# Optimization experiments

Measured on AMD Instinct MI355X. Metric: run time of the kernel, lower is better.

## Reference

```python
import jax, jax.numpy as jnp
import numpy as np

NODE_DIM, HIDDEN, PROJ = 5, 128, 256
NUM_MP = 3
BOX = 1.0


def _knn_edges(positions, k, box_length=BOX):
    """Periodic kNN graph. positions: (B,N,3) -> (src, dst) global flat indices, E = B*N*k."""
    B, N, _ = positions.shape

    def per_batch(pos):  # (N,3)
        delta = jnp.abs(pos[:, None, :] - pos[None, :, :])          # (N,N,3)
        delta = jnp.where(delta > 0.5 * box_length, box_length - delta, delta)
        dist = jnp.sqrt(jnp.sum(delta * delta, axis=-1) + 1e-12)    # (N,N)
        _, idx = jax.lax.top_k(-dist, k + 1)                        # k+1 smallest
        return idx[:, 1:]                                           # drop self -> (N,k)

    nbrs = jax.vmap(per_batch)(positions)                           # (B,N,k)
    offset = (jnp.arange(B) * N)[:, None, None]
    src = jnp.broadcast_to(jnp.arange(N)[None, :, None], (B, N, k)) + offset
    dst = nbrs + offset
    return src.reshape(-1), dst.reshape(-1)


def setup_inputs() -> dict:
    key = jax.random.key(0)
    ks = jax.random.split(key, 16)
    B, N = 8, 2048
    s = 0.05
    inp = {
        "x": jax.random.normal(ks[0], (B, N, NODE_DIM), jnp.float32),
        "positions": jax.random.uniform(ks[1], (B, N, 3), jnp.float32),
        "k": 16,
        # encoder: Linear(5,128)+ReLU, Linear(128,128)+ReLU
        "enc_w0": jax.random.normal(ks[2], (NODE_DIM, HIDDEN), jnp.float32) * s,
        "enc_b0": jnp.zeros((HIDDEN,), jnp.float32),
        "enc_w1": jax.random.normal(ks[3], (HIDDEN, HIDDEN), jnp.float32) * s,
        "enc_b1": jnp.zeros((HIDDEN,), jnp.float32),
        # message nets: Linear(2H,H)+ReLU per round
        "msg_w": jax.random.normal(ks[4], (NUM_MP, 2 * HIDDEN, HIDDEN), jnp.float32) * s,
        "msg_b": jnp.zeros((NUM_MP, HIDDEN), jnp.float32),
        # update nets: Linear(2H,H)+ReLU per round
        "upd_w": jax.random.normal(ks[5], (NUM_MP, 2 * HIDDEN, HIDDEN), jnp.float32) * s,
        "upd_b": jnp.zeros((NUM_MP, HIDDEN), jnp.float32),
        # projection head: Linear(H,H)+ReLU, Linear(H,proj)
        "proj_w0": jax.random.normal(ks[6], (HIDDEN, HIDDEN), jnp.float32) * s,
        "proj_b0": jnp.zeros((HIDDEN,), jnp.float32),
        "proj_w1": jax.random.normal(ks[7], (HIDDEN, PROJ), jnp.float32) * s,
        "proj_b1": jnp.zeros((PROJ,), jnp.float32),
    }
    return inp


def reference(x, positions, k, enc_w0, enc_b0, enc_w1, enc_b1,
              msg_w, msg_b, upd_w, upd_b, proj_w0, proj_b0, proj_w1, proj_b1):
    B, N, _ = x.shape
    BN = B * N
    relu = jax.nn.relu

    # encoder over flattened nodes
    h = relu(x.reshape(BN, -1) @ enc_w0 + enc_b0)
    h = relu(h @ enc_w1 + enc_b1)

    src, dst = _knn_edges(positions, k)
    E = src.shape[0]
    deg = jax.ops.segment_sum(jnp.ones((E,), h.dtype), dst, num_segments=BN)
    inv_deg = 1.0 / jnp.clip(deg, 1.0)

    for i in range(NUM_MP):
        # per-edge message: concat(sender, receiver) -> Linear+ReLU
        msg = relu(jnp.concatenate([h[src], h[dst]], axis=-1) @ msg_w[i] + msg_b[i])
        # mean aggregation at destination nodes
        agg = jax.ops.segment_sum(msg, dst, num_segments=BN) * inv_deg[:, None]
        # residual update
        h = h + relu(jnp.concatenate([h, agg], axis=-1) @ upd_w[i] + upd_b[i])

    z = relu(h @ proj_w0 + proj_b0) @ proj_w1 + proj_b1
    return z.reshape(B, N, PROJ), h.reshape(B, N, HIDDEN)
```

## Files before the change

kernel.cpp:

```cpp
#include <hip/hip_runtime.h>
#include <stdint.h>
#include <math.h>

#define NN 2048
#define BB 8
#define BN (BB*NN)
#define KK 16
#define EE (BN*KK)
#define HID 128
#define PROJ_D 256
#define QPB 16
#define CDIM 6
#define NCELL (CDIM*CDIM*CDIM)
#define CAP 768

typedef unsigned long long u64;
typedef unsigned short ushort_t;
typedef __attribute__((ext_vector_type(8))) short short8;
typedef __attribute__((ext_vector_type(4))) float f32x4;

__device__ __forceinline__ u64 wave_min_u64(u64 v) {
  #pragma unroll
  for (int off = 32; off > 0; off >>= 1) {
    u64 o = __shfl_xor(v, off);
    v = o < v ? o : v;
  }
  return v;
}

__global__ __launch_bounds__(256) void cellsort_kernel(
    const float* __restrict__ pos, float4* __restrict__ spos,
    int* __restrict__ cptr, int4* __restrict__ cntz) {
  __shared__ int hist[NCELL];
  __shared__ int base[NCELL];
  const int b = blockIdx.x, tid = threadIdx.x;
  #pragma unroll
  for (int k = 0; k < 4; k++)
    cntz[(b * 256 + tid) + k * 2048] = make_int4(0, 0, 0, 0);
  if (tid < NCELL) hist[tid] = 0;
  __syncthreads();
  int cellv[8];
  float4 pv[8];
  #pragma unroll
  for (int k = 0; k < 8; k++) {
    int j = tid * 8 + k;
    const float* pp = pos + ((size_t)b * NN + j) * 3;
    float x = pp[0], y = pp[1], z = pp[2];
    int cx = (int)(x * 6.0f); cx = cx > 5 ? 5 : cx;
    int cy = (int)(y * 6.0f); cy = cy > 5 ? 5 : cy;
    int cz = (int)(z * 6.0f); cz = cz > 5 ? 5 : cz;
    int cell = (cx * 6 + cy) * 6 + cz;
    cellv[k] = cell;
    pv[k] = make_float4(x, y, z, __int_as_float(j));
    atomicAdd(&hist[cell], 1);
  }
  __syncthreads();
  if (tid == 0) {
    int run = 0;
    for (int c = 0; c < NCELL; c++) {
      cptr[b * (NCELL + 1) + c] = run;
      base[c] = run;
      run += hist[c];
    }
    cptr[b * (NCELL + 1) + NCELL] = run;
  }
  __syncthreads();
  if (tid < NCELL) hist[tid] = 0;
  __syncthreads();
  #pragma unroll
  for (int k = 0; k < 8; k++) {
    int slot = base[cellv[k]] + atomicAdd(&hist[cellv[k]], 1);
    spos[(size_t)b * NN + slot] = pv[k];
  }
}

__global__ __launch_bounds__(1024) void knn_kernel(
    const float4* __restrict__ spos, const int* __restrict__ cptr,
    int* __restrict__ nbr, int* __restrict__ cnt) {
  __shared__ float4 Ps[NN];
  __shared__ unsigned Hist[QPB * 256];
  __shared__ ushort_t Cand[QPB * CAP];
  __shared__ int Cp[NCELL + 1];
  const int b  = blockIdx.x >> 7;
  const int qb = blockIdx.x & 127;
  const int wave = threadIdx.x >> 6;
  const int lane = threadIdx.x & 63;
  const int s_q = qb * QPB + wave;

  for (int t = threadIdx.x; t < NN; t += 1024)
    Ps[t] = spos[(size_t)b * NN + t];
  if (threadIdx.x <= NCELL)
    Cp[threadIdx.x] = cptr[b * (NCELL + 1) + threadIdx.x];
  __syncthreads();

  const float4 q = Ps[s_q];
  const float xi = q.x, yi = q.y, zi = q.z;
  const int orig_i = __float_as_int(q.w);
  unsigned* H = &Hist[wave * 256];
  ushort_t* CL = &Cand[wave * CAP];

  int cx = (int)(xi * 6.0f); cx = cx > 5 ? 5 : cx;
  int cy = (int)(yi * 6.0f); cy = cy > 5 ? 5 : cy;
  int cz = (int)(zi * 6.0f); cz = cz > 5 ? 5 : cz;

  int T = 0;
  bool ovf = false;
  #pragma unroll 1
  for (int dxy = 0; dxy < 9; dxy++) {
    int dx = dxy / 3 - 1, dy = dxy - (dxy / 3) * 3 - 1;
    int ncx = cx + dx; ncx += (ncx < 0) ? 6 : 0; ncx -= (ncx >= 6) ? 6 : 0;
    int ncy = cy + dy; ncy += (ncy < 0) ? 6 : 0; ncy -= (ncy >= 6) ? 6 : 0;
    int cbse = (ncx * 6 + ncy) * 6;
    int s0, l0, s1 = 0, l1 = 0;
    if (cz == 0) {
      s0 = Cp[cbse + 5]; l0 = Cp[cbse + 6] - s0;
      s1 = Cp[cbse];     l1 = Cp[cbse + 2] - s1;
    } else if (cz == 5) {
      s0 = Cp[cbse + 4]; l0 = Cp[cbse + 6] - s0;
      s1 = Cp[cbse];     l1 = Cp[cbse + 1] - s1;
    } else {
      s0 = Cp[cbse + cz - 1]; l0 = Cp[cbse + cz + 2] - s0;
    }
    if (T + l0 + l1 > CAP) { ovf = true; break; }
    for (int t = lane; t < l0; t += 64) CL[T + t] = (ushort_t)(s0 + t);
    T += l0;
    for (int t = lane; t < l1; t += 64) CL[T + t] = (ushort_t)(s1 + t);
    T += l1;
  }

  int mode = ovf ? 1 : 0;
  float scale = 1536.0f;
  int T2 = T, binmax = 254;
  int bstar = 0; unsigned C = 0;
  for (;;) {
    scale = mode ? 256.0f : 1536.0f;
    T2 = mode ? NN : T;
    binmax = mode ? 256 : 254;
    *(uint4*)&H[lane * 4] = make_uint4(0u, 0u, 0u, 0u);
    for (int t = lane; t < T2; t += 64) {
      int p = mode ? t : (int)CL[t];
      float4 pj = Ps[p];
      float tx = xi - pj.x, ty = yi - pj.y, tz = zi - pj.z;
      float ddx = __fsub_rn(tx, rintf(tx));
      float ddy = __fsub_rn(ty, rintf(ty));
      float ddz = __fsub_rn(tz, rintf(tz));
      float s = __fadd_rn(__fadd_rn(__fadd_rn(__fmul_rn(ddx,ddx), __fmul_rn(ddy,ddy)),
                                    __fmul_rn(ddz,ddz)), 1e-12f);
      float d = __fsqrt_rn(s);
      int bin = (int)(d * scale);
      if (bin < binmax) atomicAdd(&H[bin], 1u);
    }
    uint4 cv = *(const uint4*)&H[lane * 4];
    unsigned s4 = cv.x + cv.y + cv.z + cv.w;
    unsigned incl = s4;
    #pragma unroll
    for (int off = 1; off < 64; off <<= 1) {
      unsigned v = __shfl_up(incl, off);
      if (lane >= off) incl += v;
    }
    unsigned total = __shfl(incl, 63);
    if (total >= 17u) {
      unsigned base = incl - s4;
      bool has = (incl >= 17u) && (base < 17u);
      u64 hmask = __ballot(has);
      int srcl = __ffsll((unsigned long long)hmask) - 1;
      int bl = 0; unsigned Cl = 0;
      if (has) {
        if (base + cv.x >= 17u)                    { bl = lane*4 + 0; Cl = base; }
        else if (base + cv.x + cv.y >= 17u)        { bl = lane*4 + 1; Cl = base + cv.x; }
        else if (base + cv.x + cv.y + cv.z >= 17u) { bl = lane*4 + 2; Cl = base + cv.x + cv.y; }
        else                                       { bl = lane*4 + 3; Cl = base + cv.x + cv.y + cv.z; }
      }
      bstar = __shfl(bl, srcl);
      C     = __shfl(Cl, srcl);
      break;
    }
    mode = 1;
  }
  const int m = 17 - (int)C;

  u64 lst[6];
  #pragma unroll
  for (int t = 0; t < 6; t++) lst[t] = ~0ull;
  for (int t = lane; t < T2; t += 64) {
    int p = mode ? t : (int)CL[t];
    float4 pj = Ps[p];
    float tx = xi - pj.x, ty = yi - pj.y, tz = zi - pj.z;
    float ddx = __fsub_rn(tx, rintf(tx));
    float ddy = __fsub_rn(ty, rintf(ty));
    float ddz = __fsub_rn(tz, rintf(tz));
    float s = __fadd_rn(__fadd_rn(__fadd_rn(__fmul_rn(ddx,ddx), __fmul_rn(ddy,ddy)),
                                  __fmul_rn(ddz,ddz)), 1e-12f);
    float d = __fsqrt_rn(s);
    int bin = (int)(d * scale);
    if (bin == bstar) {
      u64 key = ((u64)__float_as_uint(d) << 11) | (unsigned)__float_as_int(pj.w);
      if (key < lst[5]) {
        lst[5] = key;
        #pragma unroll
        for (int u = 5; u > 0; u--) {
          u64 a = lst[u-1], c2 = lst[u];
          lst[u-1] = a < c2 ? a : c2;
          lst[u]   = a < c2 ? c2 : a;
        }
      }
    }
  }

  u64 kstar = 0;
  #pragma unroll 1
  for (int r = 0; r < m; r++) {
    u64 h0 = lst[0];
    u64 gm = wave_min_u64(h0);
    kstar = gm;
    bool win = (h0 == gm);
    #pragma unroll
    for (int u = 0; u < 5; u++) lst[u] = win ? lst[u+1] : lst[u];
    lst[5] = win ? ~0ull : lst[5];
  }

  int* outp = nbr + ((size_t)b * NN + orig_i) * KK;
  int total_e = 0;
  for (int t0 = 0; t0 < T2; t0 += 64) {
    int t = t0 + lane;
    bool pred = false;
    int oj = 0;
    if (t < T2) {
      int p = mode ? t : (int)CL[t];
      float4 pj = Ps[p];
      float tx = xi - pj.x, ty = yi - pj.y, tz = zi - pj.z;
      float ddx = __fsub_rn(tx, rintf(tx));
      float ddy = __fsub_rn(ty, rintf(ty));
      float ddz = __fsub_rn(tz, rintf(tz));
      float s = __fadd_rn(__fadd_rn(__fadd_rn(__fmul_rn(ddx,ddx), __fmul_rn(ddy,ddy)),
                                    __fmul_rn(ddz,ddz)), 1e-12f);
      float d = __fsqrt_rn(s);
      oj = __float_as_int(pj.w);
      u64 key = ((u64)__float_as_uint(d) << 11) | (unsigned)oj;
      pred = (key <= kstar) && (oj != orig_i);
    }
    u64 msk = __ballot(pred);
    if (pred) {
      int ofs = total_e + __popcll(msk & ((1ull << lane) - 1ull));
      outp[ofs] = b * NN + oj;
      atomicAdd(&cnt[b * NN + oj], 1);
    }
    total_e += __popcll(msk);
  }
}

__global__ __launch_bounds__(256) void scan_kernel(const int* __restrict__ cnt,
                                                   int* __restrict__ row_ptr) {
  __shared__ int ps[256];
  int t = threadIdx.x;
  const int4* cv = (const int4*)(cnt + t * 64);
  int4 c[16];
  int s = 0;
  #pragma unroll
  for (int i = 0; i < 16; i++) {
    c[i] = cv[i];
    s += c[i].x + c[i].y + c[i].z + c[i].w;
  }
  ps[t] = s;
  __syncthreads();
  for (int off = 1; off < 256; off <<= 1) {
    int v = 0;
    if (t >= off) v = ps[t - off];
    __syncthreads();
    ps[t] += v;
    __syncthreads();
  }
  int run = t ? ps[t - 1] : 0;
  int4* rp = (int4*)(row_ptr + t * 64);
  #pragma unroll
  for (int i = 0; i < 16; i++) {
    int4 o;
    o.x = run; run += c[i].x;
    o.y = run; run += c[i].y;
    o.z = run; run += c[i].z;
    o.w = run; run += c[i].w;
    rp[i] = o;
  }
  if (t == 255) row_ptr[BN] = run;
}

__global__ __launch_bounds__(256) void fill_kernel(const int* __restrict__ nbr,
                                                   const int* __restrict__ row_ptr,
                                                   int* __restrict__ fill,
                                                   int* __restrict__ col) {
  int e = blockIdx.x * 256 + threadIdx.x;
  int d = nbr[e];
  int srcn = e >> 4;
  int p = row_ptr[d] + atomicAdd(&fill[d], 1);
  col[p] = srcn;
}

__device__ __forceinline__ ushort_t bf16_rne(float x) {
  unsigned u = __float_as_uint(x);
  unsigned r = u + 0x7FFFu + ((u >> 16) & 1u);
  return (ushort_t)(r >> 16);
}
__device__ __forceinline__ float bf16_to_f(ushort_t h) {
  return __uint_as_float(((unsigned)h) << 16);
}
__device__ __forceinline__ unsigned cvtpk_bf16(float a, float b) {
  unsigned r;
  asm("v_cvt_pk_bf16_f32 %0, %1, %2" : "=v"(r) : "v"(a), "v"(b));
  return r;
}

__device__ __forceinline__ void cvt8(const float4 f0, const float4 f1,
                                     short8& hi, short8& lo) {
  unsigned h0 = cvtpk_bf16(f0.x, f0.y);
  unsigned h1 = cvtpk_bf16(f0.z, f0.w);
  unsigned h2 = cvtpk_bf16(f1.x, f1.y);
  unsigned h3 = cvtpk_bf16(f1.z, f1.w);
  unsigned l0 = cvtpk_bf16(f0.x - __uint_as_float(h0 << 16),
                           f0.y - __uint_as_float(h0 & 0xffff0000u));
  unsigned l1 = cvtpk_bf16(f0.z - __uint_as_float(h1 << 16),
                           f0.w - __uint_as_float(h1 & 0xffff0000u));
  unsigned l2 = cvtpk_bf16(f1.x - __uint_as_float(h2 << 16),
                           f1.y - __uint_as_float(h2 & 0xffff0000u));
  unsigned l3 = cvtpk_bf16(f1.z - __uint_as_float(h3 << 16),
                           f1.w - __uint_as_float(h3 & 0xffff0000u));
  union { unsigned u[4]; short8 v; } H, L;
  H.u[0] = h0; H.u[1] = h1; H.u[2] = h2; H.u[3] = h3;
  L.u[0] = l0; L.u[1] = l1; L.u[2] = l2; L.u[3] = l3;
  hi = H.v;
  lo = L.v;
}

__global__ __launch_bounds__(256) void prep_w_kernel(
    const float* __restrict__ enc_w1, const float* __restrict__ msg_w,
    const float* __restrict__ upd_w, const float* __restrict__ proj_w0,
    const float* __restrict__ proj_w1, ushort_t* __restrict__ wfrag) {
  int u = blockIdx.x >> 3;
  int c = (blockIdx.x & 7) * 256 + threadIdx.x;
  const float* src;
  int ldW = HID;
  if (u == 0) src = enc_w1;
  else if (u <= 6)  { int i = (u-1)>>1; int hf = (u-1)&1; src = msg_w + ((size_t)i*256 + hf*128) * HID; }
  else if (u <= 12) { int i = (u-7)>>1; int hf = (u-7)&1; src = upd_w + ((size_t)i*256 + hf*128) * HID; }
  else if (u == 13) src = proj_w0;
  else { src = proj_w1 + (u - 14) * 128; ldW = PROJ_D; }

  int ks = c >> 9, ct = (c >> 6) & 7, lane = c & 63;
  int colc = ct * 16 + (lane & 15);
  int k0 = ks * 32 + ((lane >> 4) << 3);
  float f[8];
  #pragma unroll
  for (int e = 0; e < 8; e++) f[e] = src[(size_t)(k0 + e) * ldW + colc];
  short8 hv, lv;
  cvt8(make_float4(f[0],f[1],f[2],f[3]), make_float4(f[4],f[5],f[6],f[7]), hv, lv);
  *(short8*)&wfrag[(size_t)u * 32768 + (size_t)c * 8] = hv;
  *(short8*)&wfrag[(size_t)u * 32768 + 16384 + (size_t)c * 8] = lv;
}

__device__ __forceinline__ void stage_A_convert(ushort_t* Ahi, ushort_t* Alo,
                                                const float* A, int m0, int tid) {
  #pragma unroll
  for (int i = 0; i < 4; i++) {
    int c = tid + i * 256;
    int row = c >> 4, kg = c & 15;
    const float4* ap = (const float4*)(A + (((size_t)m0 + row) << 7) + (kg << 3));
    short8 hv, lv;
    cvt8(ap[0], ap[1], hv, lv);
    int idx = (((row >> 4) * 4 + (kg >> 2)) * 64 + ((row & 15) | ((kg & 3) << 4))) * 8;
    *(short8*)&Ahi[idx] = hv;
    *(short8*)&Alo[idx] = lv;
  }
}

__device__ __forceinline__ void unit_mfma(f32x4 acc[8], const ushort_t* wf,
                                          const ushort_t* Ahi, const ushort_t* Alo,
                                          ushort_t* Bhi, ushort_t* Blo,
                                          int tid, int lane, int wid) {
  #pragma unroll 1
  for (int half = 0; half < 2; half++) {
    __syncthreads();
    const short8* ghi = (const short8*)(wf + half * 8192);
    const short8* glo = (const short8*)(wf + 16384 + half * 8192);
    #pragma unroll
    for (int i = 0; i < 4; i++) {
      ((short8*)Bhi)[tid + i * 256] = ghi[tid + i * 256];
      ((short8*)Blo)[tid + i * 256] = glo[tid + i * 256];
    }
    __syncthreads();
    #pragma unroll
    for (int ks2 = 0; ks2 < 2; ks2++) {
      int ksA = half * 2 + ks2;
      short8 ah = *(const short8*)&Ahi[((wid * 4 + ksA) * 64 + lane) * 8];
      short8 al = *(const short8*)&Alo[((wid * 4 + ksA) * 64 + lane) * 8];
      #pragma unroll
      for (int ct = 0; ct < 8; ct++) {
        short8 bh = *(const short8*)&Bhi[((ks2 * 8 + ct) * 64 + lane) * 8];
        short8 bl = *(const short8*)&Blo[((ks2 * 8 + ct) * 64 + lane) * 8];
        acc[ct] = __builtin_amdgcn_mfma_f32_16x16x32_bf16(ah, bh, acc[ct], 0, 0, 0);
        acc[ct] = __builtin_amdgcn_mfma_f32_16x16x32_bf16(ah, bl, acc[ct], 0, 0, 0);
        acc[ct] = __builtin_amdgcn_mfma_f32_16x16x32_bf16(al, bh, acc[ct], 0, 0, 0);
      }
    }
  }
}

__device__ __forceinline__ void unit_mfma_h(f32x4 acc[4], const ushort_t* wf,
                                            int ct0,
                                            const ushort_t* Ahi, const ushort_t* Alo,
                                            ushort_t* Bhi, ushort_t* Blo,
                                            int tid, int lane, int wid) {
  #pragma unroll 1
  for (int half = 0; half < 2; half++) {
    __syncthreads();
    #pragma unroll
    for (int i = 0; i < 2; i++) {
      int sc = tid + i * 256;
      int ks2 = sc >> 8;
      int cts = (sc >> 6) & 3;
      int ln  = sc & 63;
      int c = half * 1024 + ks2 * 512 + (ct0 + cts) * 64 + ln;
      ((short8*)Bhi)[sc] = *(const short8*)&wf[(size_t)c * 8];
      ((short8*)Blo)[sc] = *(const short8*)&wf[16384 + (size_t)c * 8];
    }
    __syncthreads();
    #pragma unroll
    for (int ks2 = 0; ks2 < 2; ks2++) {
      int ksA = half * 2 + ks2;
      short8 ah = *(const short8*)&Ahi[((wid * 4 + ksA) * 64 + lane) * 8];
      short8 al = *(const short8*)&Alo[((wid * 4 + ksA) * 64 + lane) * 8];
      #pragma unroll
      for (int ct = 0; ct < 4; ct++) {
        short8 bh = *(const short8*)&Bhi[((ks2 * 4 + ct) * 64 + lane) * 8];
        short8 bl = *(const short8*)&Blo[((ks2 * 4 + ct) * 64 + lane) * 8];
        acc[ct] = __builtin_amdgcn_mfma_f32_16x16x32_bf16(ah, bh, acc[ct], 0, 0, 0);
        acc[ct] = __builtin_amdgcn_mfma_f32_16x16x32_bf16(ah, bl, acc[ct], 0, 0, 0);
        acc[ct] = __builtin_amdgcn_mfma_f32_16x16x32_bf16(al, bh, acc[ct], 0, 0, 0);
      }
    }
  }
}

__global__ __launch_bounds__(256, 4) void encg1_kernel(
    const float* __restrict__ x, const float* __restrict__ ew0,
    const float* __restrict__ eb0, const ushort_t* __restrict__ wf,
    const float* __restrict__ eb1, float* __restrict__ hOut) {
  __shared__ ushort_t Ahi[8192], Alo[8192], Bhi[4096], Blo[4096];
  __shared__ float XW[1088];
  const int tid = threadIdx.x, lane = tid & 63, wid = tid >> 6;
  const int m0 = blockIdx.x * 64, ct0 = blockIdx.y * 4;

  if (tid < 80) ((float4*)XW)[tid] = ((const float4*)(x + (size_t)m0 * 5))[tid];
  else if (tid < 240) ((float4*)XW)[tid] = ((const float4*)ew0)[tid - 80];
  else {
    int k = tid - 240;
    ((float4*)XW)[240 + k] = ((const float4*)eb0)[k];
    ((float4*)XW)[256 + k] = ((const float4*)eb0)[16 + k];
  }
  __syncthreads();

  #pragma unroll
  for (int i = 0; i < 4; i++) {
    int c = tid + i * 256;
    int row = c >> 4, kg = c & 15;
    float xr[5];
    #pragma unroll
    for (int d = 0; d < 5; d++) xr[d] = XW[row * 5 + d];
    float v[8];
    #pragma unroll
    for (int e = 0; e < 8; e++) {
      int col = kg * 8 + e;
      float a = XW[960 + col];
      #pragma unroll
      for (int d = 0; d < 5; d++) a += xr[d] * XW[320 + d * 128 + col];
      v[e] = fmaxf(a, 0.f);
    }
    short8 hv, lv;
    cvt8(make_float4(v[0],v[1],v[2],v[3]), make_float4(v[4],v[5],v[6],v[7]), hv, lv);
    int idx = (((row >> 4) * 4 + (kg >> 2)) * 64 + ((row & 15) | ((kg & 3) << 4))) * 8;
    *(short8*)&Ahi[idx] = hv;
    *(short8*)&Alo[idx] = lv;
  }

  f32x4 acc[4];
  f32x4 z = {0.f, 0.f, 0.f, 0.f};
  #pragma unroll
  for (int ct = 0; ct < 4; ct++) acc[ct] = z;
  unit_mfma_h(acc, wf, ct0, Ahi, Alo, Bhi, Blo, tid, lane, wid);

  const int rbase = m0 + wid * 16 + ((lane >> 4) << 2);
  const int cb = lane & 15;
  #pragma unroll
  for (int ct = 0; ct < 4; ct++) {
    int n = (ct0 + ct) * 16 + cb;
    float bv = eb1[n];
    #pragma unroll
    for (int r = 0; r < 4; r++)
      hOut[(size_t)(rbase + r) * HID + n] = fmaxf(acc[ct][r] + bv, 0.f);
  }
}

template<int RELU>
__global__ __launch_bounds__(256, 4) void g1_kernel(
    const float* __restrict__ A, const ushort_t* __restrict__ wf,
    const float* __restrict__ bias, float* __restrict__ out) {
  __shared__ ushort_t Ahi[8192], Alo[8192], Bhi[4096], Blo[4096];
  const int tid = threadIdx.x, lane = tid & 63, wid = tid >> 6;
  const int m0 = blockIdx.x * 64, ct0 = blockIdx.y * 4;
  stage_A_convert(Ahi, Alo, A, m0, tid);
  f32x4 acc[4];
  f32x4 z = {0.f, 0.f, 0.f, 0.f};
  #pragma unroll
  for (int ct = 0; ct < 4; ct++) acc[ct] = z;
  unit_mfma_h(acc, wf, ct0, Ahi, Alo, Bhi, Blo, tid, lane, wid);

  const int rbase = m0 + wid * 16 + ((lane >> 4) << 2);
  const int cb = lane & 15;
  #pragma unroll
  for (int ct = 0; ct < 4; ct++) {
    int n = (ct0 + ct) * 16 + cb;
    float bv = bias ? bias[n] : 0.f;
    #pragma unroll
    for (int r = 0; r < 4; r++) {
      float v = acc[ct][r] + bv;
      if (RELU) v = fmaxf(v, 0.f);
      out[(size_t)(rbase + r) * HID + n] = v;
    }
  }
}

__global__ __launch_bounds__(256, 4) void msg_kernel(
    const float* __restrict__ h, const ushort_t* __restrict__ wfT,
    const ushort_t* __restrict__ wfB, const float* __restrict__ mb,
    ushort_t* __restrict__ bufA, ushort_t* __restrict__ bufB) {
  __shared__ ushort_t Ahi[8192], Alo[8192], Bhi[8192], Blo[8192];
  const int tid = threadIdx.x, lane = tid & 63, wid = tid >> 6;
  const int m0 = blockIdx.x * 64;
  const int y = blockIdx.y;
  stage_A_convert(Ahi, Alo, h, m0, tid);
  f32x4 acc[8];
  f32x4 z = {0.f, 0.f, 0.f, 0.f};
  #pragma unroll
  for (int ct = 0; ct < 8; ct++) acc[ct] = z;
  unit_mfma(acc, y ? wfB : wfT, Ahi, Alo, Bhi, Blo, tid, lane, wid);

  ushort_t* out = y ? bufB : bufA;
  const float* bias = y ? mb : nullptr;
  const int rbase = m0 + wid * 16 + ((lane >> 4) << 2);
  const int cb = lane & 15;
  #pragma unroll
  for (int ct = 0; ct < 8; ct++) {
    int n = ct * 16 + cb;
    float bv = bias ? bias[n] : 0.f;
    #pragma unroll
    for (int r = 0; r < 4; r++)
      out[(size_t)(rbase + r) * HID + n] = bf16_rne(acc[ct][r] + bv);
  }
}

__global__ __launch_bounds__(256, 4) void upd_kernel(
    const float* __restrict__ h, const ushort_t* __restrict__ wuT,
    const float* __restrict__ aggF, const ushort_t* __restrict__ wuB,
    const float* __restrict__ ub, float* __restrict__ out) {
  __shared__ ushort_t Ahi[8192], Alo[8192], Bhi[4096], Blo[4096];
  const int tid = threadIdx.x, lane = tid & 63, wid = tid >> 6;
  const int m0 = blockIdx.x * 64, ct0 = blockIdx.y * 4;
  stage_A_convert(Ahi, Alo, h, m0, tid);
  f32x4 acc[4];
  f32x4 z = {0.f, 0.f, 0.f, 0.f};
  #pragma unroll
  for (int ct = 0; ct < 4; ct++) acc[ct] = z;
  unit_mfma_h(acc, wuT, ct0, Ahi, Alo, Bhi, Blo, tid, lane, wid);
  __syncthreads();
  stage_A_convert(Ahi, Alo, aggF, m0, tid);
  unit_mfma_h(acc, wuB, ct0, Ahi, Alo, Bhi, Blo, tid, lane, wid);

  const int rbase = m0 + wid * 16 + ((lane >> 4) << 2);
  const int cb = lane & 15;
  #pragma unroll
  for (int ct = 0; ct < 4; ct++) {
    int n = (ct0 + ct) * 16 + cb;
    float bv = ub[n];
    #pragma unroll
    for (int r = 0; r < 4; r++) {
      float v = fmaxf(acc[ct][r] + bv, 0.f)
              + h[(size_t)(rbase + r) * HID + n];
      out[(size_t)(rbase + r) * HID + n] = v;
    }
  }
}

__global__ __launch_bounds__(256, 4) void proj1_kernel(
    const float* __restrict__ A, const ushort_t* __restrict__ wf01,
    const float* __restrict__ pb1, float* __restrict__ zout) {
  __shared__ ushort_t Ahi[8192], Alo[8192], Bhi[8192], Blo[8192];
  const int tid = threadIdx.x, lane = tid & 63, wid = tid >> 6;
  const int m0 = blockIdx.x * 64;
  const int y = blockIdx.y;
  stage_A_convert(Ahi, Alo, A, m0, tid);
  f32x4 acc[8];
  f32x4 z = {0.f, 0.f, 0.f, 0.f};
  #pragma unroll
  for (int ct = 0; ct < 8; ct++) acc[ct] = z;
  unit_mfma(acc, wf01 + (size_t)y * 32768, Ahi, Alo, Bhi, Blo, tid, lane, wid);

  const int rbase = m0 + wid * 16 + ((lane >> 4) << 2);
  const int cb = lane & 15;
  #pragma unroll
  for (int ct = 0; ct < 8; ct++) {
    int n = y * 128 + ct * 16 + cb;
    float bv = pb1[n];
    #pragma unroll
    for (int r = 0; r < 4; r++)
      zout[(size_t)(rbase + r) * PROJ_D + n] = acc[ct][r] + bv;
  }
}

__global__ __launch_bounds__(256) void agg_kernel(const ushort_t* __restrict__ Abuf,
                                                  const ushort_t* __restrict__ Bbuf,
                                                  const int* __restrict__ row_ptr,
                                                  const int* __restrict__ col,
                                                  float* __restrict__ agg) {
  int j = blockIdx.x * 2 + (threadIdx.x >> 7);
  int c = threadIdx.x & 127;
  float bj = bf16_to_f(Bbuf[(size_t)j * HID + c]);
  int s = row_ptr[j], e = row_ptr[j + 1];
  float acc = 0.f;
  int p = s;
  for (; p + 4 <= e; p += 4) {
    int i0 = col[p], i1 = col[p+1], i2 = col[p+2], i3 = col[p+3];
    float v0 = bf16_to_f(Abuf[(size_t)i0 * HID + c]);
    float v1 = bf16_to_f(Abuf[(size_t)i1 * HID + c]);
    float v2 = bf16_to_f(Abuf[(size_t)i2 * HID + c]);
    float v3 = bf16_to_f(Abuf[(size_t)i3 * HID + c]);
    acc += fmaxf(v0 + bj, 0.f) + fmaxf(v1 + bj, 0.f)
         + fmaxf(v2 + bj, 0.f) + fmaxf(v3 + bj, 0.f);
  }
  for (; p < e; p++) {
    int i = col[p];
    acc += fmaxf(bf16_to_f(Abuf[(size_t)i * HID + c]) + bj, 0.f);
  }
  float deg = (float)(e - s);
  float inv = 1.0f / fmaxf(deg, 1.0f);
  agg[(size_t)j * HID + c] = acc * inv;
}

extern "C" void kernel_launch(void* const* d_in, const int* in_sizes, int n_in,
                              void* d_out, int out_size, void* d_ws, size_t ws_size,
                              hipStream_t stream) {
  (void)in_sizes; (void)n_in; (void)out_size; (void)ws_size;
  const float* x       = (const float*)d_in[0];
  const float* pos     = (const float*)d_in[1];
  const float* enc_w0  = (const float*)d_in[3];
  const float* enc_b0  = (const float*)d_in[4];
  const float* enc_w1  = (const float*)d_in[5];
  const float* enc_b1  = (const float*)d_in[6];
  const float* msg_w   = (const float*)d_in[7];
  const float* msg_b   = (const float*)d_in[8];
  const float* upd_w   = (const float*)d_in[9];
  const float* upd_b   = (const float*)d_in[10];
  const float* proj_w0 = (const float*)d_in[11];
  const float* proj_b0 = (const float*)d_in[12];
  const float* proj_w1 = (const float*)d_in[13];
  const float* proj_b1 = (const float*)d_in[14];

  char* ws = (char*)d_ws;
  size_t off = 0;
  auto alloc = [&](size_t bytes) -> void* {
    void* p = ws + off;
    off += (bytes + 255) & ~(size_t)255;
    return p;
  };
  int*      nbr     = (int*)alloc((size_t)EE * 4);
  int*      cnt     = (int*)alloc((size_t)BN * 4);
  int*      fill    = (int*)alloc((size_t)BN * 4);
  int*      row_ptr = (int*)alloc((size_t)(BN + 1) * 4);
  int*      col     = (int*)alloc((size_t)EE * 4);
  float*    h_a     = (float*)alloc((size_t)BN * HID * 4);
  float*    h_b     = (float*)alloc((size_t)BN * HID * 4);
  ushort_t* bufA    = (ushort_t*)alloc((size_t)BN * HID * 2);
  ushort_t* bufB    = (ushort_t*)alloc((size_t)BN * HID * 2);
  float*    bufAgg  = (float*)alloc((size_t)BN * HID * 4);
  ushort_t* wfrag   = (ushort_t*)alloc((size_t)16 * 32768 * 2);
  float4*   spos    = (float4*)alloc((size_t)BN * 16);
  int*      cptr    = (int*)alloc((size_t)BB * (NCELL + 1) * 4);
  float*    out     = (float*)d_out;
  float*    hOut    = out + (size_t)BN * PROJ_D;

  cellsort_kernel<<<BB, 256, 0, stream>>>(pos, spos, cptr, (int4*)cnt);
  prep_w_kernel<<<128, 256, 0, stream>>>(enc_w1, msg_w, upd_w, proj_w0, proj_w1, wfrag);
  knn_kernel<<<BN / QPB, 1024, 0, stream>>>(spos, cptr, nbr, cnt);
  scan_kernel<<<1, 256, 0, stream>>>(cnt, row_ptr);
  fill_kernel<<<EE / 256, 256, 0, stream>>>(nbr, row_ptr, fill, col);

  encg1_kernel<<<dim3(BN / 64, 2), 256, 0, stream>>>(
      x, enc_w0, enc_b0, wfrag + 0 * 32768, enc_b1, h_a);

  float* hc = h_a;
  float* hn = h_b;
  for (int i = 0; i < 3; i++) {
    msg_kernel<<<dim3(BN / 64, 2), 256, 0, stream>>>(
        hc, wfrag + (size_t)(1 + 2 * i) * 32768,
        wfrag + (size_t)(2 + 2 * i) * 32768, msg_b + (size_t)i * HID,
        bufA, bufB);
    agg_kernel<<<BN / 2, 256, 0, stream>>>(bufA, bufB, row_ptr, col, bufAgg);
    float* target = (i == 2) ? hOut : hn;
    upd_kernel<<<dim3(BN / 64, 2), 256, 0, stream>>>(
        hc, wfrag + (size_t)(7 + 2 * i) * 32768, bufAgg,
        wfrag + (size_t)(8 + 2 * i) * 32768, upd_b + (size_t)i * HID, target);
    hn = hc; hc = target;
  }

  g1_kernel<1><<<dim3(BN / 64, 2), 256, 0, stream>>>(hc, wfrag + 13 * 32768,
                                                     proj_b0, h_b);
  proj1_kernel<<<dim3(BN / 64, 2), 256, 0, stream>>>(
      h_b, wfrag + 14 * 32768, proj_b1, out);
}
```

Measured before the change: 214.1 us.

## Cache kNN candidate distances in registers and merge setup kernels

The kNN kernel now computes each candidate's periodic distance once and keeps it, with the neighbour index, in per-lane registers (up to 8 per lane). The histogram, bucket selection and output passes reuse these values instead of recomputing distances three times. The candidate capacity drops from 768 to 512 to fit the register array, so queries with more candidates fall back to the slower all-pairs path more often. Cell sorting and weight-fragment preparation are also merged into one launch, saving a kernel launch.

```diff
diff --git a/kernel.cpp b/kernel.cpp
--- a/kernel.cpp
+++ b/kernel.cpp
@@ -12,7 +12,7 @@
 #define QPB 16
 #define CDIM 6
 #define NCELL (CDIM*CDIM*CDIM)
-#define CAP 768
+#define CAP 512
 
 typedef unsigned long long u64;
 typedef unsigned short ushort_t;
@@ -26,273 +26,6 @@
     v = o < v ? o : v;
   }
   return v;
-}
-
-__global__ __launch_bounds__(256) void cellsort_kernel(
-    const float* __restrict__ pos, float4* __restrict__ spos,
-    int* __restrict__ cptr, int4* __restrict__ cntz) {
-  __shared__ int hist[NCELL];
-  __shared__ int base[NCELL];
-  const int b = blockIdx.x, tid = threadIdx.x;
-  #pragma unroll
-  for (int k = 0; k < 4; k++)
-    cntz[(b * 256 + tid) + k * 2048] = make_int4(0, 0, 0, 0);
-  if (tid < NCELL) hist[tid] = 0;
-  __syncthreads();
-  int cellv[8];
-  float4 pv[8];
-  #pragma unroll
-  for (int k = 0; k < 8; k++) {
-    int j = tid * 8 + k;
-    const float* pp = pos + ((size_t)b * NN + j) * 3;
-    float x = pp[0], y = pp[1], z = pp[2];
-    int cx = (int)(x * 6.0f); cx = cx > 5 ? 5 : cx;
-    int cy = (int)(y * 6.0f); cy = cy > 5 ? 5 : cy;
-    int cz = (int)(z * 6.0f); cz = cz > 5 ? 5 : cz;
-    int cell = (cx * 6 + cy) * 6 + cz;
-    cellv[k] = cell;
-    pv[k] = make_float4(x, y, z, __int_as_float(j));
-    atomicAdd(&hist[cell], 1);
-  }
-  __syncthreads();
-  if (tid == 0) {
-    int run = 0;
-    for (int c = 0; c < NCELL; c++) {
-      cptr[b * (NCELL + 1) + c] = run;
-      base[c] = run;
-      run += hist[c];
-    }
-    cptr[b * (NCELL + 1) + NCELL] = run;
-  }
-  __syncthreads();
-  if (tid < NCELL) hist[tid] = 0;
-  __syncthreads();
-  #pragma unroll
-  for (int k = 0; k < 8; k++) {
-    int slot = base[cellv[k]] + atomicAdd(&hist[cellv[k]], 1);
-    spos[(size_t)b * NN + slot] = pv[k];
-  }
-}
-
-__global__ __launch_bounds__(1024) void knn_kernel(
-    const float4* __restrict__ spos, const int* __restrict__ cptr,
-    int* __restrict__ nbr, int* __restrict__ cnt) {
-  __shared__ float4 Ps[NN];
-  __shared__ unsigned Hist[QPB * 256];
-  __shared__ ushort_t Cand[QPB * CAP];
-  __shared__ int Cp[NCELL + 1];
-  const int b  = blockIdx.x >> 7;
-  const int qb = blockIdx.x & 127;
-  const int wave = threadIdx.x >> 6;
-  const int lane = threadIdx.x & 63;
-  const int s_q = qb * QPB + wave;
-
-  for (int t = threadIdx.x; t < NN; t += 1024)
-    Ps[t] = spos[(size_t)b * NN + t];
-  if (threadIdx.x <= NCELL)
-    Cp[threadIdx.x] = cptr[b * (NCELL + 1) + threadIdx.x];
-  __syncthreads();
-
-  const float4 q = Ps[s_q];
-  const float xi = q.x, yi = q.y, zi = q.z;
-  const int orig_i = __float_as_int(q.w);
-  unsigned* H = &Hist[wave * 256];
-  ushort_t* CL = &Cand[wave * CAP];
-
-  int cx = (int)(xi * 6.0f); cx = cx > 5 ? 5 : cx;
-  int cy = (int)(yi * 6.0f); cy = cy > 5 ? 5 : cy;
-  int cz = (int)(zi * 6.0f); cz = cz > 5 ? 5 : cz;
-
-  int T = 0;
-  bool ovf = false;
-  #pragma unroll 1
-  for (int dxy = 0; dxy < 9; dxy++) {
-    int dx = dxy / 3 - 1, dy = dxy - (dxy / 3) * 3 - 1;
-    int ncx = cx + dx; ncx += (ncx < 0) ? 6 : 0; ncx -= (ncx >= 6) ? 6 : 0;
-    int ncy = cy + dy; ncy += (ncy < 0) ? 6 : 0; ncy -= (ncy >= 6) ? 6 : 0;
-    int cbse = (ncx * 6 + ncy) * 6;
-    int s0, l0, s1 = 0, l1 = 0;
-    if (cz == 0) {
-      s0 = Cp[cbse + 5]; l0 = Cp[cbse + 6] - s0;
-      s1 = Cp[cbse];     l1 = Cp[cbse + 2] - s1;
-    } else if (cz == 5) {
-      s0 = Cp[cbse + 4]; l0 = Cp[cbse + 6] - s0;
-      s1 = Cp[cbse];     l1 = Cp[cbse + 1] - s1;
-    } else {
-      s0 = Cp[cbse + cz - 1]; l0 = Cp[cbse + cz + 2] - s0;
-    }
-    if (T + l0 + l1 > CAP) { ovf = true; break; }
-    for (int t = lane; t < l0; t += 64) CL[T + t] = (ushort_t)(s0 + t);
-    T += l0;
-    for (int t = lane; t < l1; t += 64) CL[T + t] = (ushort_t)(s1 + t);
-    T += l1;
-  }
-
-  int mode = ovf ? 1 : 0;
-  float scale = 1536.0f;
-  int T2 = T, binmax = 254;
-  int bstar = 0; unsigned C = 0;
-  for (;;) {
-    scale = mode ? 256.0f : 1536.0f;
-    T2 = mode ? NN : T;
-    binmax = mode ? 256 : 254;
-    *(uint4*)&H[lane * 4] = make_uint4(0u, 0u, 0u, 0u);
-    for (int t = lane; t < T2; t += 64) {
-      int p = mode ? t : (int)CL[t];
-      float4 pj = Ps[p];
-      float tx = xi - pj.x, ty = yi - pj.y, tz = zi - pj.z;
-      float ddx = __fsub_rn(tx, rintf(tx));
-      float ddy = __fsub_rn(ty, rintf(ty));
-      float ddz = __fsub_rn(tz, rintf(tz));
-      float s = __fadd_rn(__fadd_rn(__fadd_rn(__fmul_rn(ddx,ddx), __fmul_rn(ddy,ddy)),
-                                    __fmul_rn(ddz,ddz)), 1e-12f);
-      float d = __fsqrt_rn(s);
-      int bin = (int)(d * scale);
-      if (bin < binmax) atomicAdd(&H[bin], 1u);
-    }
-    uint4 cv = *(const uint4*)&H[lane * 4];
-    unsigned s4 = cv.x + cv.y + cv.z + cv.w;
-    unsigned incl = s4;
-    #pragma unroll
-    for (int off = 1; off < 64; off <<= 1) {
-      unsigned v = __shfl_up(incl, off);
-      if (lane >= off) incl += v;
-    }
-    unsigned total = __shfl(incl, 63);
-    if (total >= 17u) {
-      unsigned base = incl - s4;
-      bool has = (incl >= 17u) && (base < 17u);
-      u64 hmask = __ballot(has);
-      int srcl = __ffsll((unsigned long long)hmask) - 1;
-      int bl = 0; unsigned Cl = 0;
-      if (has) {
-        if (base + cv.x >= 17u)                    { bl = lane*4 + 0; Cl = base; }
-        else if (base + cv.x + cv.y >= 17u)        { bl = lane*4 + 1; Cl = base + cv.x; }
-        else if (base + cv.x + cv.y + cv.z >= 17u) { bl = lane*4 + 2; Cl = base + cv.x + cv.y; }
-        else                                       { bl = lane*4 + 3; Cl = base + cv.x + cv.y + cv.z; }
-      }
-      bstar = __shfl(bl, srcl);
-      C     = __shfl(Cl, srcl);
-      break;
-    }
-    mode = 1;
-  }
-  const int m = 17 - (int)C;
-
-  u64 lst[6];
-  #pragma unroll
-  for (int t = 0; t < 6; t++) lst[t] = ~0ull;
-  for (int t = lane; t < T2; t += 64) {
-    int p = mode ? t : (int)CL[t];
-    float4 pj = Ps[p];
-    float tx = xi - pj.x, ty = yi - pj.y, tz = zi - pj.z;
-    float ddx = __fsub_rn(tx, rintf(tx));
-    float ddy = __fsub_rn(ty, rintf(ty));
-    float ddz = __fsub_rn(tz, rintf(tz));
-    float s = __fadd_rn(__fadd_rn(__fadd_rn(__fmul_rn(ddx,ddx), __fmul_rn(ddy,ddy)),
-                                  __fmul_rn(ddz,ddz)), 1e-12f);
-    float d = __fsqrt_rn(s);
-    int bin = (int)(d * scale);
-    if (bin == bstar) {
-      u64 key = ((u64)__float_as_uint(d) << 11) | (unsigned)__float_as_int(pj.w);
-      if (key < lst[5]) {
-        lst[5] = key;
-        #pragma unroll
-        for (int u = 5; u > 0; u--) {
-          u64 a = lst[u-1], c2 = lst[u];
-          lst[u-1] = a < c2 ? a : c2;
-          lst[u]   = a < c2 ? c2 : a;
-        }
-      }
-    }
-  }
-
-  u64 kstar = 0;
-  #pragma unroll 1
-  for (int r = 0; r < m; r++) {
-    u64 h0 = lst[0];
-    u64 gm = wave_min_u64(h0);
-    kstar = gm;
-    bool win = (h0 == gm);
-    #pragma unroll
-    for (int u = 0; u < 5; u++) lst[u] = win ? lst[u+1] : lst[u];
-    lst[5] = win ? ~0ull : lst[5];
-  }
-
-  int* outp = nbr + ((size_t)b * NN + orig_i) * KK;
-  int total_e = 0;
-  for (int t0 = 0; t0 < T2; t0 += 64) {
-    int t = t0 + lane;
-    bool pred = false;
-    int oj = 0;
-    if (t < T2) {
-      int p = mode ? t : (int)CL[t];
-      float4 pj = Ps[p];
-      float tx = xi - pj.x, ty = yi - pj.y, tz = zi - pj.z;
-      float ddx = __fsub_rn(tx, rintf(tx));
-      float ddy = __fsub_rn(ty, rintf(ty));
-      float ddz = __fsub_rn(tz, rintf(tz));
-      float s = __fadd_rn(__fadd_rn(__fadd_rn(__fmul_rn(ddx,ddx), __fmul_rn(ddy,ddy)),
-                                    __fmul_rn(ddz,ddz)), 1e-12f);
-      float d = __fsqrt_rn(s);
-      oj = __float_as_int(pj.w);
-      u64 key = ((u64)__float_as_uint(d) << 11) | (unsigned)oj;
-      pred = (key <= kstar) && (oj != orig_i);
-    }
-    u64 msk = __ballot(pred);
-    if (pred) {
-      int ofs = total_e + __popcll(msk & ((1ull << lane) - 1ull));
-      outp[ofs] = b * NN + oj;
-      atomicAdd(&cnt[b * NN + oj], 1);
-    }
-    total_e += __popcll(msk);
-  }
-}
-
-__global__ __launch_bounds__(256) void scan_kernel(const int* __restrict__ cnt,
-                                                   int* __restrict__ row_ptr) {
-  __shared__ int ps[256];
-  int t = threadIdx.x;
-  const int4* cv = (const int4*)(cnt + t * 64);
-  int4 c[16];
-  int s = 0;
-  #pragma unroll
-  for (int i = 0; i < 16; i++) {
-    c[i] = cv[i];
-    s += c[i].x + c[i].y + c[i].z + c[i].w;
-  }
-  ps[t] = s;
-  __syncthreads();
-  for (int off = 1; off < 256; off <<= 1) {
-    int v = 0;
-    if (t >= off) v = ps[t - off];
-    __syncthreads();
-    ps[t] += v;
-    __syncthreads();
-  }
-  int run = t ? ps[t - 1] : 0;
-  int4* rp = (int4*)(row_ptr + t * 64);
-  #pragma unroll
-  for (int i = 0; i < 16; i++) {
-    int4 o;
-    o.x = run; run += c[i].x;
-    o.y = run; run += c[i].y;
-    o.z = run; run += c[i].z;
-    o.w = run; run += c[i].w;
-    rp[i] = o;
-  }
-  if (t == 255) row_ptr[BN] = run;
-}
-
-__global__ __launch_bounds__(256) void fill_kernel(const int* __restrict__ nbr,
-                                                   const int* __restrict__ row_ptr,
-                                                   int* __restrict__ fill,
-                                                   int* __restrict__ col) {
-  int e = blockIdx.x * 256 + threadIdx.x;
-  int d = nbr[e];
-  int srcn = e >> 4;
-  int p = row_ptr[d] + atomicAdd(&fill[d], 1);
-  col[p] = srcn;
 }
 
 __device__ __forceinline__ ushort_t bf16_rne(float x) {
@@ -330,30 +63,361 @@
   lo = L.v;
 }
 
-__global__ __launch_bounds__(256) void prep_w_kernel(
+__global__ __launch_bounds__(256) void setup_kernel(
+    const float* __restrict__ pos, float4* __restrict__ spos,
+    int* __restrict__ cptr, int4* __restrict__ cntz,
     const float* __restrict__ enc_w1, const float* __restrict__ msg_w,
     const float* __restrict__ upd_w, const float* __restrict__ proj_w0,
     const float* __restrict__ proj_w1, ushort_t* __restrict__ wfrag) {
-  int u = blockIdx.x >> 3;
-  int c = (blockIdx.x & 7) * 256 + threadIdx.x;
-  const float* src;
-  int ldW = HID;
-  if (u == 0) src = enc_w1;
-  else if (u <= 6)  { int i = (u-1)>>1; int hf = (u-1)&1; src = msg_w + ((size_t)i*256 + hf*128) * HID; }
-  else if (u <= 12) { int i = (u-7)>>1; int hf = (u-7)&1; src = upd_w + ((size_t)i*256 + hf*128) * HID; }
-  else if (u == 13) src = proj_w0;
-  else { src = proj_w1 + (u - 14) * 128; ldW = PROJ_D; }
-
-  int ks = c >> 9, ct = (c >> 6) & 7, lane = c & 63;
-  int colc = ct * 16 + (lane & 15);
-  int k0 = ks * 32 + ((lane >> 4) << 3);
-  float f[8];
-  #pragma unroll
-  for (int e = 0; e < 8; e++) f[e] = src[(size_t)(k0 + e) * ldW + colc];
-  short8 hv, lv;
-  cvt8(make_float4(f[0],f[1],f[2],f[3]), make_float4(f[4],f[5],f[6],f[7]), hv, lv);
-  *(short8*)&wfrag[(size_t)u * 32768 + (size_t)c * 8] = hv;
-  *(short8*)&wfrag[(size_t)u * 32768 + 16384 + (size_t)c * 8] = lv;
+  __shared__ int hist[NCELL];
+  __shared__ int base[NCELL];
+  const int tid = threadIdx.x;
+  if (blockIdx.x < 8) {
+    const int b = blockIdx.x;
+    #pragma unroll
+    for (int k = 0; k < 4; k++)
+      cntz[(b * 256 + tid) + k * 2048] = make_int4(0, 0, 0, 0);
+    if (tid < NCELL) hist[tid] = 0;
+    __syncthreads();
+    int cellv[8];
+    float4 pv[8];
+    #pragma unroll
+    for (int k = 0; k < 8; k++) {
+      int j = tid * 8 + k;
+      const float* pp = pos + ((size_t)b * NN + j) * 3;
+      float x = pp[0], y = pp[1], z = pp[2];
+      int cx = (int)(x * 6.0f); cx = cx > 5 ? 5 : cx;
+      int cy = (int)(y * 6.0f); cy = cy > 5 ? 5 : cy;
+      int cz = (int)(z * 6.0f); cz = cz > 5 ? 5 : cz;
+      int cell = (cx * 6 + cy) * 6 + cz;
+      cellv[k] = cell;
+      pv[k] = make_float4(x, y, z, __int_as_float(j));
+      atomicAdd(&hist[cell], 1);
+    }
+    __syncthreads();
+    if (tid == 0) {
+      int run = 0;
+      for (int c = 0; c < NCELL; c++) {
+        cptr[b * (NCELL + 1) + c] = run;
+        base[c] = run;
+        run += hist[c];
+      }
+      cptr[b * (NCELL + 1) + NCELL] = run;
+    }
+    __syncthreads();
+    if (tid < NCELL) hist[tid] = 0;
+    __syncthreads();
+    #pragma unroll
+    for (int k = 0; k < 8; k++) {
+      int slot = base[cellv[k]] + atomicAdd(&hist[cellv[k]], 1);
+      spos[(size_t)b * NN + slot] = pv[k];
+    }
+  } else {
+    int ub = blockIdx.x - 8;
+    int u = ub >> 3;
+    int c = (ub & 7) * 256 + tid;
+    const float* src;
+    int ldW = HID;
+    if (u == 0) src = enc_w1;
+    else if (u <= 6)  { int i = (u-1)>>1; int hf = (u-1)&1; src = msg_w + ((size_t)i*256 + hf*128) * HID; }
+    else if (u <= 12) { int i = (u-7)>>1; int hf = (u-7)&1; src = upd_w + ((size_t)i*256 + hf*128) * HID; }
+    else if (u == 13) src = proj_w0;
+    else { src = proj_w1 + (u - 14) * 128; ldW = PROJ_D; }
+    int ks = c >> 9, ct = (c >> 6) & 7, lane = c & 63;
+    int colc = ct * 16 + (lane & 15);
+    int k0 = ks * 32 + ((lane >> 4) << 3);
+    float f[8];
+    #pragma unroll
+    for (int e = 0; e < 8; e++) f[e] = src[(size_t)(k0 + e) * ldW + colc];
+    short8 hv, lv;
+    cvt8(make_float4(f[0],f[1],f[2],f[3]), make_float4(f[4],f[5],f[6],f[7]), hv, lv);
+    *(short8*)&wfrag[(size_t)u * 32768 + (size_t)c * 8] = hv;
+    *(short8*)&wfrag[(size_t)u * 32768 + 16384 + (size_t)c * 8] = lv;
+  }
+}
+
+__global__ __launch_bounds__(1024) void knn_kernel(
+    const float4* __restrict__ spos, const int* __restrict__ cptr,
+    int* __restrict__ nbr, int* __restrict__ cnt) {
+  __shared__ float4 Ps[NN];
+  __shared__ unsigned Hist[QPB * 256];
+  __shared__ ushort_t Cand[QPB * CAP];
+  __shared__ int Cp[NCELL + 1];
+  const int b  = blockIdx.x >> 7;
+  const int qb = blockIdx.x & 127;
+  const int wave = threadIdx.x >> 6;
+  const int lane = threadIdx.x & 63;
+  const int s_q = qb * QPB + wave;
+
+  for (int t = threadIdx.x; t < NN; t += 1024)
+    Ps[t] = spos[(size_t)b * NN + t];
+  if (threadIdx.x <= NCELL)
+    Cp[threadIdx.x] = cptr[b * (NCELL + 1) + threadIdx.x];
+  __syncthreads();
+
+  const float4 q = Ps[s_q];
+  const float xi = q.x, yi = q.y, zi = q.z;
+  const int orig_i = __float_as_int(q.w);
+  unsigned* H = &Hist[wave * 256];
+  ushort_t* CL = &Cand[wave * CAP];
+
+  int cx = (int)(xi * 6.0f); cx = cx > 5 ? 5 : cx;
+  int cy = (int)(yi * 6.0f); cy = cy > 5 ? 5 : cy;
+  int cz = (int)(zi * 6.0f); cz = cz > 5 ? 5 : cz;
+
+  int T = 0;
+  bool ovf = false;
+  #pragma unroll 1
+  for (int dxy = 0; dxy < 9; dxy++) {
+    int dx = dxy / 3 - 1, dy = dxy - (dxy / 3) * 3 - 1;
+    int ncx = cx + dx; ncx += (ncx < 0) ? 6 : 0; ncx -= (ncx >= 6) ? 6 : 0;
+    int ncy = cy + dy; ncy += (ncy < 0) ? 6 : 0; ncy -= (ncy >= 6) ? 6 : 0;
+    int cbse = (ncx * 6 + ncy) * 6;
+    int s0, l0, s1 = 0, l1 = 0;
+    if (cz == 0) {
+      s0 = Cp[cbse + 5]; l0 = Cp[cbse + 6] - s0;
+      s1 = Cp[cbse];     l1 = Cp[cbse + 2] - s1;
+    } else if (cz == 5) {
+      s0 = Cp[cbse + 4]; l0 = Cp[cbse + 6] - s0;
+      s1 = Cp[cbse];     l1 = Cp[cbse + 1] - s1;
+    } else {
+      s0 = Cp[cbse + cz - 1]; l0 = Cp[cbse + cz + 2] - s0;
+    }
+    if (T + l0 + l1 > CAP) { ovf = true; break; }
+    for (int t = lane; t < l0; t += 64) CL[T + t] = (ushort_t)(s0 + t);
+    T += l0;
+    for (int t = lane; t < l1; t += 64) CL[T + t] = (ushort_t)(s1 + t);
+    T += l1;
+  }
+
+  int mode = ovf ? 1 : 0;
+
+  float dreg[8];
+  int ojreg[8];
+  if (!mode) {
+    #pragma unroll
+    for (int it = 0; it < 8; it++) {
+      int t = it * 64 + lane;
+      float d = 1e30f;
+      int oj = 0;
+      if (t < T) {
+        float4 pj = Ps[(int)CL[t]];
+        float tx = xi - pj.x, ty = yi - pj.y, tz = zi - pj.z;
+        float ddx = __fsub_rn(tx, rintf(tx));
+        float ddy = __fsub_rn(ty, rintf(ty));
+        float ddz = __fsub_rn(tz, rintf(tz));
+        float s = __fadd_rn(__fadd_rn(__fadd_rn(__fmul_rn(ddx,ddx), __fmul_rn(ddy,ddy)),
+                                      __fmul_rn(ddz,ddz)), 1e-12f);
+        d = __fsqrt_rn(s);
+        oj = __float_as_int(pj.w);
+      }
+      dreg[it] = d;
+      ojreg[it] = oj;
+    }
+  }
+
+  float scale = 1536.0f;
+  int bstar = 0; unsigned C = 0;
+  for (;;) {
+    scale = mode ? 256.0f : 1536.0f;
+    int binmax = mode ? 256 : 254;
+    *(uint4*)&H[lane * 4] = make_uint4(0u, 0u, 0u, 0u);
+    if (!mode) {
+      #pragma unroll
+      for (int it = 0; it < 8; it++) {
+        int bin = (int)(dreg[it] * 1536.0f);
+        if (bin < binmax) atomicAdd(&H[bin], 1u);
+      }
+    } else {
+      for (int t = lane; t < NN; t += 64) {
+        float4 pj = Ps[t];
+        float tx = xi - pj.x, ty = yi - pj.y, tz = zi - pj.z;
+        float ddx = __fsub_rn(tx, rintf(tx));
+        float ddy = __fsub_rn(ty, rintf(ty));
+        float ddz = __fsub_rn(tz, rintf(tz));
+        float s = __fadd_rn(__fadd_rn(__fadd_rn(__fmul_rn(ddx,ddx), __fmul_rn(ddy,ddy)),
+                                      __fmul_rn(ddz,ddz)), 1e-12f);
+        float d = __fsqrt_rn(s);
+        int bin = (int)(d * 256.0f);
+        if (bin < 256) atomicAdd(&H[bin], 1u);
+      }
+    }
+    uint4 cv = *(const uint4*)&H[lane * 4];
+    unsigned s4 = cv.x + cv.y + cv.z + cv.w;
+    unsigned incl = s4;
+    #pragma unroll
+    for (int off = 1; off < 64; off <<= 1) {
+      unsigned v = __shfl_up(incl, off);
+      if (lane >= off) incl += v;
+    }
+    unsigned total = __shfl(incl, 63);
+    if (total >= 17u) {
+      unsigned base = incl - s4;
+      bool has = (incl >= 17u) && (base < 17u);
+      u64 hmask = __ballot(has);
+      int srcl = __ffsll((unsigned long long)hmask) - 1;
+      int bl = 0; unsigned Cl = 0;
+      if (has) {
+        if (base + cv.x >= 17u)                    { bl = lane*4 + 0; Cl = base; }
+        else if (base + cv.x + cv.y >= 17u)        { bl = lane*4 + 1; Cl = base + cv.x; }
+        else if (base + cv.x + cv.y + cv.z >= 17u) { bl = lane*4 + 2; Cl = base + cv.x + cv.y; }
+        else                                       { bl = lane*4 + 3; Cl = base + cv.x + cv.y + cv.z; }
+      }
+      bstar = __shfl(bl, srcl);
+      C     = __shfl(Cl, srcl);
+      break;
+    }
+    mode = 1;
+  }
+  const int m = 17 - (int)C;
+
+  u64 lst[6];
+  #pragma unroll
+  for (int t = 0; t < 6; t++) lst[t] = ~0ull;
+  if (!mode) {
+    #pragma unroll
+    for (int it = 0; it < 8; it++) {
+      int bin = (int)(dreg[it] * 1536.0f);
+      if (bin == bstar) {
+        u64 key = ((u64)__float_as_uint(dreg[it]) << 11) | (unsigned)ojreg[it];
+        if (key < lst[5]) {
+          lst[5] = key;
+          #pragma unroll
+          for (int u = 5; u > 0; u--) {
+            u64 a = lst[u-1], c2 = lst[u];
+            lst[u-1] = a < c2 ? a : c2;
+            lst[u]   = a < c2 ? c2 : a;
+          }
+        }
+      }
+    }
+  } else {
+    for (int t = lane; t < NN; t += 64) {
+      float4 pj = Ps[t];
+      float tx = xi - pj.x, ty = yi - pj.y, tz = zi - pj.z;
+      float ddx = __fsub_rn(tx, rintf(tx));
+      float ddy = __fsub_rn(ty, rintf(ty));
+      float ddz = __fsub_rn(tz, rintf(tz));
+      float s = __fadd_rn(__fadd_rn(__fadd_rn(__fmul_rn(ddx,ddx), __fmul_rn(ddy,ddy)),
+                                    __fmul_rn(ddz,ddz)), 1e-12f);
+      float d = __fsqrt_rn(s);
+      int bin = (int)(d * 256.0f);
+      if (bin == bstar) {
+        u64 key = ((u64)__float_as_uint(d) << 11) | (unsigned)__float_as_int(pj.w);
+        if (key < lst[5]) {
+          lst[5] = key;
+          #pragma unroll
+          for (int u = 5; u > 0; u--) {
+            u64 a = lst[u-1], c2 = lst[u];
+            lst[u-1] = a < c2 ? a : c2;
+            lst[u]   = a < c2 ? c2 : a;
+          }
+        }
+      }
+    }
+  }
+
+  u64 kstar = 0;
+  #pragma unroll 1
+  for (int r = 0; r < m; r++) {
+    u64 h0 = lst[0];
+    u64 gm = wave_min_u64(h0);
+    kstar = gm;
+    bool win = (h0 == gm);
+    #pragma unroll
+    for (int u = 0; u < 5; u++) lst[u] = win ? lst[u+1] : lst[u];
+    lst[5] = win ? ~0ull : lst[5];
+  }
+
+  int* outp = nbr + ((size_t)b * NN + orig_i) * KK;
+  int total_e = 0;
+  if (!mode) {
+    #pragma unroll
+    for (int it = 0; it < 8; it++) {
+      int t = it * 64 + lane;
+      int oj = ojreg[it];
+      bool pred = false;
+      if (t < T) {
+        u64 key = ((u64)__float_as_uint(dreg[it]) << 11) | (unsigned)oj;
+        pred = (key <= kstar) && (oj != orig_i);
+      }
+      u64 msk = __ballot(pred);
+      if (pred) {
+        int ofs = total_e + __popcll(msk & ((1ull << lane) - 1ull));
+        outp[ofs] = b * NN + oj;
+        atomicAdd(&cnt[b * NN + oj], 1);
+      }
+      total_e += __popcll(msk);
+    }
+  } else {
+    for (int t0 = 0; t0 < NN; t0 += 64) {
+      int t = t0 + lane;
+      float4 pj = Ps[t];
+      float tx = xi - pj.x, ty = yi - pj.y, tz = zi - pj.z;
+      float ddx = __fsub_rn(tx, rintf(tx));
+      float ddy = __fsub_rn(ty, rintf(ty));
+      float ddz = __fsub_rn(tz, rintf(tz));
+      float s = __fadd_rn(__fadd_rn(__fadd_rn(__fmul_rn(ddx,ddx), __fmul_rn(ddy,ddy)),
+                                    __fmul_rn(ddz,ddz)), 1e-12f);
+      float d = __fsqrt_rn(s);
+      int oj = __float_as_int(pj.w);
+      u64 key = ((u64)__float_as_uint(d) << 11) | (unsigned)oj;
+      bool pred = (key <= kstar) && (oj != orig_i);
+      u64 msk = __ballot(pred);
+      if (pred) {
+        int ofs = total_e + __popcll(msk & ((1ull << lane) - 1ull));
+        outp[ofs] = b * NN + oj;
+        atomicAdd(&cnt[b * NN + oj], 1);
+      }
+      total_e += __popcll(msk);
+    }
+  }
+}
+
+__global__ __launch_bounds__(256) void scan_kernel(const int* __restrict__ cnt,
+                                                   int* __restrict__ row_ptr) {
+  __shared__ int ps[256];
+  int t = threadIdx.x;
+  const int4* cv = (const int4*)(cnt + t * 64);
+  int4 c[16];
+  int s = 0;
+  #pragma unroll
+  for (int i = 0; i < 16; i++) {
+    c[i] = cv[i];
+    s += c[i].x + c[i].y + c[i].z + c[i].w;
+  }
+  ps[t] = s;
+  __syncthreads();
+  for (int off = 1; off < 256; off <<= 1) {
+    int v = 0;
+    if (t >= off) v = ps[t - off];
+    __syncthreads();
+    ps[t] += v;
+    __syncthreads();
+  }
+  int run = t ? ps[t - 1] : 0;
+  int4* rp = (int4*)(row_ptr + t * 64);
+  #pragma unroll
+  for (int i = 0; i < 16; i++) {
+    int4 o;
+    o.x = run; run += c[i].x;
+    o.y = run; run += c[i].y;
+    o.z = run; run += c[i].z;
+    o.w = run; run += c[i].w;
+    rp[i] = o;
+  }
+  if (t == 255) row_ptr[BN] = run;
+}
+
+__global__ __launch_bounds__(256) void fill_kernel(const int* __restrict__ nbr,
+                                                   const int* __restrict__ row_ptr,
+                                                   int* __restrict__ fill,
+                                                   int* __restrict__ col) {
+  int e = blockIdx.x * 256 + threadIdx.x;
+  int d = nbr[e];
+  int srcn = e >> 4;
+  int p = row_ptr[d] + atomicAdd(&fill[d], 1);
+  col[p] = srcn;
 }
 
 __device__ __forceinline__ void stage_A_convert(ushort_t* Ahi, ushort_t* Alo,
@@ -685,8 +749,9 @@
   float*    out     = (float*)d_out;
   float*    hOut    = out + (size_t)BN * PROJ_D;
 
-  cellsort_kernel<<<BB, 256, 0, stream>>>(pos, spos, cptr, (int4*)cnt);
-  prep_w_kernel<<<128, 256, 0, stream>>>(enc_w1, msg_w, upd_w, proj_w0, proj_w1, wfrag);
+  setup_kernel<<<136, 256, 0, stream>>>(pos, spos, cptr, (int4*)cnt,
+                                        enc_w1, msg_w, upd_w, proj_w0, proj_w1,
+                                        wfrag);
   knn_kernel<<<BN / QPB, 1024, 0, stream>>>(spos, cptr, nbr, cnt);
   scan_kernel<<<1, 256, 0, stream>>>(cnt, row_ptr);
   fill_kernel<<<EE / 256, 256, 0, stream>>>(nbr, row_ptr, fill, col);
```

Result: faster. 208.9 us (-2.4%).
